# Optimization experiments

Hardware: AMD Instinct MI355X
Metric: run time of the kernel (lower is better)

Reference implementation:

```python
import jax, jax.numpy as jnp
import numpy as np

# TT config: input_dimension=2048, output_multiplier=4, rank=16
# top_ranks    = [8,2,2,2,2,2,2,2,2]  (prod = 2048)
# bottom_ranks = [8,2,2,2,2,2,2,2,2]  (prod = 2048)
# core shapes (top, bottom, left, right): left/right are TT bond ranks.
CORE_SHAPES = [(8, 8, 1, 16)] + [(2, 2, 16, 16)] * 7 + [(2, 2, 16, 1)]


def setup_inputs() -> dict:
    key = jax.random.key(0)
    ks = jax.random.split(key, 10)
    inp = {"x": jax.random.normal(ks[0], (4, 2048, 2048), dtype=jnp.float32)}
    for i, s in enumerate(CORE_SHAPES):
        inp[f"p{i}"] = jax.random.normal(ks[i + 1], s, dtype=jnp.float32)
    return inp


def _tt_apply(x, ps):
    # x: [B, S, D] with D = prod(top_ranks) = 2048
    B, S, D = x.shape
    T = B * S
    # Normalize every core to (top, bottom, left_bond_in, right_bond_out).
    # Original einsum: '... abcdefghi, ajs, bkst, cltu, dmuv, envw, fowx, gpxy, hqzy, irz -> ... jklmnopqr'
    # Core 7 ('hqzy') has swapped bonds: its 4th dim (y) is the incoming bond
    # from core 6 and its 3rd dim (z) is the outgoing bond into core 8 ('irz').
    cores = list(ps[:7]) + [jnp.transpose(ps[7], (0, 1, 3, 2)), ps[8]]
    # core 0 is used as p0[:, :, 0, :] in the original; its left dim is 1 so
    # keeping the singleton left axis is identical math.
    y = x.reshape(T, 1, 1, D)  # [T, out_so_far=1, bond=1, remaining_top=D]
    J, M = 1, D
    for g in cores:
        tk, bk, lk, rk = g.shape
        y = y.reshape(T, J, lk, tk, M // tk)
        # contract incoming bond l and current top index a with the core
        y = jnp.einsum('tjlam,ablr->tjbrm', y, g)
        J *= bk
        M //= tk
        y = y.reshape(T, J, rk, M)
    # final: rk == 1, M == 1 -> [T, J] with J = prod(bottom_ranks) = 2048
    return y.reshape(B, S, J)


def reference(x, p0, p1, p2, p3, p4, p5, p6, p7, p8):
    return _tt_apply(x, (p0, p1, p2, p3, p4, p5, p6, p7, p8))
```

## Files before the change

### kernel.cpp

```cpp
#include <hip/hip_runtime.h>
#include <stdint.h>

typedef unsigned short u16;
typedef __bf16 bf16x8 __attribute__((ext_vector_type(8)));
typedef float f32x16 __attribute__((ext_vector_type(16)));
typedef u16 u16x8 __attribute__((ext_vector_type(8)));

__device__ __forceinline__ u16 f2bf(float f) {
  uint32_t u = __float_as_uint(f);
  u += 0x7fffu + ((u >> 16) & 1u);
  return (u16)(u >> 16);
}

__global__ __launch_bounds__(256) void build_lr_kernel(
    const float* __restrict__ p0, const float* __restrict__ p1,
    const float* __restrict__ p2, const float* __restrict__ p3,
    const float* __restrict__ p4, const float* __restrict__ p5,
    const float* __restrict__ p6, const float* __restrict__ p7,
    const float* __restrict__ p8, float* __restrict__ L4, float* __restrict__ R) {
  __shared__ float sA[16384];
  __shared__ float sB[4096];
  const int tid = threadIdx.x;
  if (blockIdx.x < 16) {
    for (int i = tid; i < 1024; i += 256) sA[i] = p0[i];
    __syncthreads();
    for (int i = tid; i < 4096; i += 256) {
      int r = i & 15, t = i >> 4;
      int Bb = t & 15, Aa = t >> 4;
      int a = Aa & 1, A = Aa >> 1, b = Bb & 1, B = Bb >> 1;
      const float* srow = sA + (A * 8 + B) * 16;
      const float* g = p1 + ((a * 2 + b) * 16) * 16 + r;
      float s = 0.f;
#pragma unroll
      for (int l = 0; l < 16; l++) s += srow[l] * g[l * 16];
      sB[i] = s;
    }
    __syncthreads();
    for (int i = tid; i < 16384; i += 256) {
      int r = i & 15, t = i >> 4;
      int Bb = t & 31, Aa = t >> 5;
      int a = Aa & 1, A = Aa >> 1, b = Bb & 1, B = Bb >> 1;
      const float* srow = sB + (A * 16 + B) * 16;
      const float* g = p2 + ((a * 2 + b) * 16) * 16 + r;
      float s = 0.f;
#pragma unroll
      for (int l = 0; l < 16; l++) s += srow[l] * g[l * 16];
      sA[i] = s;
    }
    __syncthreads();
    int gi = blockIdx.x * 256 + tid;
    int b3 = gi & 1, a3 = (gi >> 1) & 1;
    int B2 = (gi >> 2) & 31, A2 = gi >> 7;
    const float* srow = sA + (A2 * 32 + B2) * 16;
    const float* g3 = p3 + ((a3 * 2 + b3) * 16) * 16;
    float tmp[16];
#pragma unroll
    for (int r3 = 0; r3 < 16; r3++) {
      float s = 0.f;
#pragma unroll
      for (int r2 = 0; r2 < 16; r2++) s += srow[r2] * g3[r2 * 16 + r3];
      tmp[r3] = s;
    }
#pragma unroll
    for (int ab = 0; ab < 4; ab++) {
      int a4 = ab >> 1, b4 = ab & 1;
      const float* g4 = p4 + (ab * 16) * 16;
      int AL = A2 * 4 + a3 * 2 + a4;
      int BL = B2 * 4 + b3 * 2 + b4;
      float* drow = L4 + (AL * 128 + BL) * 16;
#pragma unroll
      for (int r4 = 0; r4 < 16; r4++) {
        float s = 0.f;
#pragma unroll
        for (int r3 = 0; r3 < 16; r3++) s += tmp[r3] * g4[r3 * 16 + r4];
        drow[r4] = s;
      }
    }
  } else {
    for (int i = tid; i < 64; i += 256) sA[i] = p8[i];
    __syncthreads();
    for (int i = tid; i < 256; i += 256) {
      int rl = i & 15, t = i >> 4;
      int Bt = t & 3, At = t >> 2;
      int a = At >> 1, Ap = At & 1, b = Bt >> 1, Bp = Bt & 1;
      const float* srow = sA + (Ap * 2 + Bp) * 16;
      const float* g = p7 + ((a * 2 + b) * 16) * 16 + rl;
      float s = 0.f;
#pragma unroll
      for (int rk = 0; rk < 16; rk++) s += srow[rk] * g[rk * 16];
      sB[i] = s;
    }
    __syncthreads();
    for (int i = tid; i < 1024; i += 256) {
      int rl = i & 15, t = i >> 4;
      int Bt = t & 7, At = t >> 3;
      int a = At >> 2, Ap = At & 3, b = Bt >> 2, Bp = Bt & 3;
      const float* srow = sB + (Ap * 4 + Bp) * 16;
      const float* g = p6 + (((a * 2 + b) * 16) + rl) * 16;
      float s = 0.f;
#pragma unroll
      for (int rk = 0; rk < 16; rk++) s += srow[rk] * g[rk];
      sA[i] = s;
    }
    __syncthreads();
    for (int i = tid; i < 4096; i += 256) {
      int rl = i & 15, t = i >> 4;
      int Bt = t & 15, At = t >> 4;
      int a = At >> 3, Ap = At & 7, b = Bt >> 3, Bp = Bt & 7;
      const float* srow = sA + (Ap * 8 + Bp) * 16;
      const float* g = p5 + (((a * 2 + b) * 16) + rl) * 16;
      float s = 0.f;
#pragma unroll
      for (int rk = 0; rk < 16; rk++) s += srow[rk] * g[rk];
      R[i] = s;
    }
  }
}

__global__ __launch_bounds__(256) void prep_kernel(const float* __restrict__ L4,
                                                   const float* __restrict__ R,
                                                   u16* __restrict__ Wt,
                                                   const float* __restrict__ x,
                                                   u16* __restrict__ xb) {
  if (blockIdx.x < 2048) {
    int t = blockIdx.x * 256 + threadIdx.x;
    int e = t * 8;
    int Af = e & 2047;
    int Bf = e >> 11;
    const float* lrow = L4 + ((Af >> 4) * 128 + (Bf >> 4)) * 16;
    float lv[16];
#pragma unroll
    for (int r = 0; r < 16; r++) lv[r] = lrow[r];
    const float* rbase = R + (Bf & 15) * 16;
    u16x8 o;
#pragma unroll
    for (int j = 0; j < 8; j++) {
      const float* rrow = rbase + ((Af + j) & 15) * 256;
      float s = 0.f;
#pragma unroll
      for (int r = 0; r < 16; r++) s += lv[r] * rrow[r];
      o[j] = f2bf(s);
    }
    *(u16x8*)(Wt + (size_t)Bf * 2048 + Af) = o;
  } else {
    size_t i = ((size_t)(blockIdx.x - 2048) * 256 + threadIdx.x) * 8;
    float4 u = *(const float4*)(x + i);
    float4 v = *(const float4*)(x + i + 4);
    u16x8 o;
    o[0] = f2bf(u.x); o[1] = f2bf(u.y); o[2] = f2bf(u.z); o[3] = f2bf(u.w);
    o[4] = f2bf(v.x); o[5] = f2bf(v.y); o[6] = f2bf(v.z); o[7] = f2bf(v.w);
    *(u16x8*)(xb + i) = o;
  }
}

#define SB0() __builtin_amdgcn_sched_barrier(0)

#define STAGE_OP(g, S, h, dsto, gk)                                            \
  __builtin_amdgcn_global_load_lds(                                            \
      (const __attribute__((address_space(1))) void*)(g[h][0] + (gk)),         \
      (__attribute__((address_space(3))) void*)(S + (dsto) + ldst), 16, 0, 0); \
  __builtin_amdgcn_global_load_lds(                                            \
      (const __attribute__((address_space(1))) void*)(g[h][1] + (gk)),         \
      (__attribute__((address_space(3))) void*)(S + (dsto) + ldst + 4096), 16, 0, 0);

#define STAGE_A(h, dsto, gk) STAGE_OP(gA, As, h, dsto, gk)
#define STAGE_B(h, dsto, gk) STAGE_OP(gB, Bs, h, dsto, gk)

#define LOAD_AF(ah, pa)                                                        \
  _Pragma("unroll") for (int m = 0; m < 2; m++)                                \
      _Pragma("unroll") for (int ks = 0; ks < 4; ks++)                         \
          af[m][ks] = *(const bf16x8*)(As + (pa) + (ah) * 8192 + rbA +         \
                                       m * 2048 + ((((ks * 2) + hl) ^ key) * 8));

#define LOAD_BV(bh, pa)                                                        \
  _Pragma("unroll") for (int ks = 0; ks < 4; ks++)                             \
      bv[ks] = *(const bf16x8*)(Bs + (pa) + (bh) * 8192 + rbB +                \
                                ((((ks * 2) + hl) ^ key) * 8));

#define MFMA8(ah, bh)                                                          \
  _Pragma("unroll") for (int ks = 0; ks < 4; ks++) {                           \
    acc[ah][bh][0] = __builtin_amdgcn_mfma_f32_32x32x16_bf16(                  \
        af[0][ks], bv[ks], acc[ah][bh][0], 0, 0, 0);                           \
    acc[ah][bh][1] = __builtin_amdgcn_mfma_f32_32x32x16_bf16(                  \
        af[1][ks], bv[ks], acc[ah][bh][1], 0, 0, 0);                           \
  }

#define PH_MID()                                                               \
  SB0();                                                                       \
  asm volatile("s_barrier" ::: "memory");                                      \
  asm volatile("s_waitcnt lgkmcnt(0)" ::: "memory");                           \
  SB0();                                                                       \
  __builtin_amdgcn_s_setprio(1);

#define PH_END()                                                               \
  __builtin_amdgcn_s_setprio(0);                                               \
  SB0();                                                                       \
  asm volatile("s_barrier" ::: "memory");                                      \
  SB0();

#define PH_END_VM()                                                            \
  __builtin_amdgcn_s_setprio(0);                                               \
  SB0();                                                                       \
  asm volatile("s_waitcnt vmcnt(6)" ::: "memory");                             \
  asm volatile("s_barrier" ::: "memory");                                      \
  SB0();

__global__ __launch_bounds__(512, 2) void gemm_kernel(const u16* __restrict__ A,
                                                      const u16* __restrict__ B,
                                                      float* __restrict__ C) {
  __shared__ alignas(128) u16 As[4 * 8192];
  __shared__ alignas(128) u16 Bs[4 * 8192];
  const int tid = threadIdx.x;
  const int lane = tid & 63;
  const int w = tid >> 6;
  const int wr = w >> 2;
  const int wc = w & 3;
  const int r32 = lane & 31;
  const int hl = lane >> 5;

  const int F = blockIdx.x + (blockIdx.y << 3);
  const int li = F >> 3;
  const int m0 = ((F & 7) * 4 + (li >> 3)) << 8;
  const int n0 = (li & 7) << 8;

  const int srow = lane >> 3;
  const int soct = (lane & 7) ^ srow;
  const u16* gA[2][2];
  const u16* gB[2][2];
#pragma unroll
  for (int h = 0; h < 2; h++)
#pragma unroll
    for (int q = 0; q < 2; q++) {
      int r = h * 128 + q * 64 + w * 8 + srow;
      gA[h][q] = A + (size_t)(m0 + r) * 2048 + soct * 8;
      gB[h][q] = B + (size_t)(n0 + r) * 2048 + soct * 8;
    }
  const int ldst = w * 512;

  const int key = r32 & 7;
  const int rbA = (wr * 64 + r32) * 64;
  const int rbB = (wc * 32 + r32) * 64;

  f32x16 acc[2][2][2] = {};
  bf16x8 af[2][4], bv[4];

  STAGE_A(0, 0, 0);      SB0();
  STAGE_B(1, 8192, 0);   SB0();
  STAGE_A(1, 8192, 0);   SB0();
  STAGE_B(0, 0, 0);      SB0();
  STAGE_A(0, 16384, 64); SB0();
  STAGE_B(1, 24576, 64); SB0();
  STAGE_A(1, 24576, 64); SB0();
  asm volatile("s_waitcnt vmcnt(6)" ::: "memory");
  asm volatile("s_barrier" ::: "memory");
  SB0();

  for (int t = 0; t < 32; t++) {
    const int pa = (t & 1) << 14;
    const int pan = 16384 - pa;
    const int k1 = (t + 1 < 32 ? t + 1 : 31) * 64;
    const int k2 = (t + 2 < 32 ? t + 2 : 31) * 64;
    LOAD_AF(0, pa);
    LOAD_BV(0, pa);
    STAGE_B(0, pan, k1);
    PH_MID();
    MFMA8(0, 0);
    PH_END();
    LOAD_BV(1, pa);
    STAGE_A(0, pa, k2);
    PH_MID();
    MFMA8(0, 1);
    PH_END();
    LOAD_AF(1, pa);
    STAGE_B(1, pa + 8192, k2);
    PH_MID();
    MFMA8(1, 1);
    PH_END();
    LOAD_BV(0, pa);
    STAGE_A(1, pa + 8192, k2);
    PH_MID();
    MFMA8(1, 0);
    PH_END_VM();
  }

  asm volatile("s_waitcnt vmcnt(0)" ::: "memory");

#pragma unroll
  for (int ah = 0; ah < 2; ah++)
#pragma unroll
    for (int bh = 0; bh < 2; bh++)
#pragma unroll
      for (int m = 0; m < 2; m++) {
        size_t cbase = (size_t)(m0 + ah * 128 + wr * 64 + m * 32 + 4 * hl) * 2048 +
                       (n0 + bh * 128 + wc * 32 + r32);
#pragma unroll
        for (int reg = 0; reg < 16; reg++) {
          int row = (reg & 3) + 8 * (reg >> 2);
          __builtin_nontemporal_store(acc[ah][bh][m][reg], C + cbase + (size_t)row * 2048);
        }
      }
}

extern "C" void kernel_launch(void* const* d_in, const int* in_sizes, int n_in,
                              void* d_out, int out_size, void* d_ws, size_t ws_size,
                              hipStream_t stream) {
  const float* x = (const float*)d_in[0];
  const float* p0 = (const float*)d_in[1];
  const float* p1 = (const float*)d_in[2];
  const float* p2 = (const float*)d_in[3];
  const float* p3 = (const float*)d_in[4];
  const float* p4 = (const float*)d_in[5];
  const float* p5 = (const float*)d_in[6];
  const float* p6 = (const float*)d_in[7];
  const float* p7 = (const float*)d_in[8];
  const float* p8 = (const float*)d_in[9];
  char* ws = (char*)d_ws;
  u16* xbf = (u16*)ws;
  u16* Wt = (u16*)(ws + 33554432);
  float* L4 = (float*)(ws + 41943040);
  float* R = (float*)(ws + 42991616);

  build_lr_kernel<<<17, 256, 0, stream>>>(p0, p1, p2, p3, p4, p5, p6, p7, p8, L4, R);
  prep_kernel<<<10240, 256, 0, stream>>>(L4, R, Wt, x, xbf);
  gemm_kernel<<<dim3(8, 32), 512, 0, stream>>>(xbf, Wt, (float*)d_out);
}
```

Before: 271.0 us.

## Restructure GEMM main loop with double-buffered B fragments and finer LDS waits

Reworks the 4-phase GEMM K-loop so B fragments are double-buffered in registers (bv0/bv1). The next tile's first B fragment is prefetched before the end-of-iteration barrier, and partial lgkmcnt waits let MFMAs start before every LDS read has returned. Per-thread global pointer arrays are replaced by one lane offset plus uniform row offsets, which should cut VGPR use and address arithmetic. This removes some barriers and full LDS drains on the critical path, at the cost of more live fragment registers and more subtle ordering requirements between the LDS reads and the async global-to-LDS stages.

```diff
diff --git a/kernel.cpp b/kernel.cpp
--- a/kernel.cpp
+++ b/kernel.cpp
@@ -154,56 +154,42 @@
 }
 
 #define SB0() __builtin_amdgcn_sched_barrier(0)
-
-#define STAGE_OP(g, S, h, dsto, gk)                                            \
+#define LGKM(n) asm volatile("s_waitcnt lgkmcnt(" #n ")" ::: "memory")
+#define VMCW(n) asm volatile("s_waitcnt vmcnt(" #n ")" ::: "memory")
+#define BAR() asm volatile("s_barrier" ::: "memory")
+
+#define STAGE1(Sbase, dsto, gp, uoff)                                          \
   __builtin_amdgcn_global_load_lds(                                            \
-      (const __attribute__((address_space(1))) void*)(g[h][0] + (gk)),         \
-      (__attribute__((address_space(3))) void*)(S + (dsto) + ldst), 16, 0, 0); \
-  __builtin_amdgcn_global_load_lds(                                            \
-      (const __attribute__((address_space(1))) void*)(g[h][1] + (gk)),         \
-      (__attribute__((address_space(3))) void*)(S + (dsto) + ldst + 4096), 16, 0, 0);
-
-#define STAGE_A(h, dsto, gk) STAGE_OP(gA, As, h, dsto, gk)
-#define STAGE_B(h, dsto, gk) STAGE_OP(gB, Bs, h, dsto, gk)
-
-#define LOAD_AF(ah, pa)                                                        \
-  _Pragma("unroll") for (int m = 0; m < 2; m++)                                \
-      _Pragma("unroll") for (int ks = 0; ks < 4; ks++)                         \
-          af[m][ks] = *(const bf16x8*)(As + (pa) + (ah) * 8192 + rbA +         \
-                                       m * 2048 + ((((ks * 2) + hl) ^ key) * 8));
-
-#define LOAD_BV(bh, pa)                                                        \
+      (const __attribute__((address_space(1))) void*)((gp) + (uoff) + pl),     \
+      (__attribute__((address_space(3))) void*)((Sbase) + (dsto) + ldst), 16, 0, 0)
+
+#define STAGE_A(h, dsto, gk)                                                   \
+  STAGE1(As, (dsto), A, uA + ((h)*128) * 2048 + (gk));                         \
+  STAGE1(As, (dsto) + 4096, A, uA + ((h)*128 + 64) * 2048 + (gk))
+
+#define STAGE_B(h, dsto, gk)                                                   \
+  STAGE1(Bs, (dsto), B, uB + ((h)*128) * 2048 + (gk));                         \
+  STAGE1(Bs, (dsto) + 4096, B, uB + ((h)*128 + 64) * 2048 + (gk))
+
+#define LOAD_AF_H(dst, ah, m, pav)                                             \
   _Pragma("unroll") for (int ks = 0; ks < 4; ks++)                             \
-      bv[ks] = *(const bf16x8*)(Bs + (pa) + (bh) * 8192 + rbB +                \
-                                ((((ks * 2) + hl) ^ key) * 8));
-
-#define MFMA8(ah, bh)                                                          \
+      dst[ks] = *(const bf16x8*)(As + (pav) + (ah)*8192 + rbA + (m)*2048 +     \
+                                 (((ks * 2 + hl) ^ key) * 8))
+
+#define LOAD_BV(dst, bh, pav)                                                  \
+  _Pragma("unroll") for (int ks = 0; ks < 4; ks++)                             \
+      dst[ks] = *(const bf16x8*)(Bs + (pav) + (bh)*8192 + rbB +                \
+                                 (((ks * 2 + hl) ^ key) * 8))
+
+#define MFMA4(afh, bvv, accv)                                                  \
+  _Pragma("unroll") for (int ks = 0; ks < 4; ks++)                             \
+      accv = __builtin_amdgcn_mfma_f32_32x32x16_bf16(afh[ks], bvv[ks], accv, 0, 0, 0)
+
+#define MFMA8I(afarr, bvv, accp)                                               \
   _Pragma("unroll") for (int ks = 0; ks < 4; ks++) {                           \
-    acc[ah][bh][0] = __builtin_amdgcn_mfma_f32_32x32x16_bf16(                  \
-        af[0][ks], bv[ks], acc[ah][bh][0], 0, 0, 0);                           \
-    acc[ah][bh][1] = __builtin_amdgcn_mfma_f32_32x32x16_bf16(                  \
-        af[1][ks], bv[ks], acc[ah][bh][1], 0, 0, 0);                           \
+    accp[0] = __builtin_amdgcn_mfma_f32_32x32x16_bf16(afarr[0][ks], bvv[ks], accp[0], 0, 0, 0); \
+    accp[1] = __builtin_amdgcn_mfma_f32_32x32x16_bf16(afarr[1][ks], bvv[ks], accp[1], 0, 0, 0); \
   }
-
-#define PH_MID()                                                               \
-  SB0();                                                                       \
-  asm volatile("s_barrier" ::: "memory");                                      \
-  asm volatile("s_waitcnt lgkmcnt(0)" ::: "memory");                           \
-  SB0();                                                                       \
-  __builtin_amdgcn_s_setprio(1);
-
-#define PH_END()                                                               \
-  __builtin_amdgcn_s_setprio(0);                                               \
-  SB0();                                                                       \
-  asm volatile("s_barrier" ::: "memory");                                      \
-  SB0();
-
-#define PH_END_VM()                                                            \
-  __builtin_amdgcn_s_setprio(0);                                               \
-  SB0();                                                                       \
-  asm volatile("s_waitcnt vmcnt(6)" ::: "memory");                             \
-  asm volatile("s_barrier" ::: "memory");                                      \
-  SB0();
 
 __global__ __launch_bounds__(512, 2) void gemm_kernel(const u16* __restrict__ A,
                                                       const u16* __restrict__ B,
@@ -225,16 +211,9 @@
 
   const int srow = lane >> 3;
   const int soct = (lane & 7) ^ srow;
-  const u16* gA[2][2];
-  const u16* gB[2][2];
-#pragma unroll
-  for (int h = 0; h < 2; h++)
-#pragma unroll
-    for (int q = 0; q < 2; q++) {
-      int r = h * 128 + q * 64 + w * 8 + srow;
-      gA[h][q] = A + (size_t)(m0 + r) * 2048 + soct * 8;
-      gB[h][q] = B + (size_t)(n0 + r) * 2048 + soct * 8;
-    }
+  const int uA = m0 * 2048;
+  const int uB = n0 * 2048;
+  const int pl = (w * 8 + srow) * 2048 + soct * 8;
   const int ldst = w * 512;
 
   const int key = r32 & 7;
@@ -242,7 +221,7 @@
   const int rbB = (wc * 32 + r32) * 64;
 
   f32x16 acc[2][2][2] = {};
-  bf16x8 af[2][4], bv[4];
+  bf16x8 af[2][4], bv0[4], bv1[4];
 
   STAGE_A(0, 0, 0);      SB0();
   STAGE_B(1, 8192, 0);   SB0();
@@ -251,39 +230,58 @@
   STAGE_A(0, 16384, 64); SB0();
   STAGE_B(1, 24576, 64); SB0();
   STAGE_A(1, 24576, 64); SB0();
-  asm volatile("s_waitcnt vmcnt(6)" ::: "memory");
-  asm volatile("s_barrier" ::: "memory");
+  VMCW(6);
+  BAR();
+  LOAD_BV(bv0, 0, 0);
   SB0();
 
+#pragma unroll 1
   for (int t = 0; t < 32; t++) {
-    const int pa = (t & 1) << 14;
-    const int pan = 16384 - pa;
-    const int k1 = (t + 1 < 32 ? t + 1 : 31) * 64;
-    const int k2 = (t + 2 < 32 ? t + 2 : 31) * 64;
-    LOAD_AF(0, pa);
-    LOAD_BV(0, pa);
-    STAGE_B(0, pan, k1);
-    PH_MID();
-    MFMA8(0, 0);
-    PH_END();
-    LOAD_BV(1, pa);
-    STAGE_A(0, pa, k2);
-    PH_MID();
-    MFMA8(0, 1);
-    PH_END();
-    LOAD_AF(1, pa);
-    STAGE_B(1, pa + 8192, k2);
-    PH_MID();
-    MFMA8(1, 1);
-    PH_END();
-    LOAD_BV(0, pa);
-    STAGE_A(1, pa + 8192, k2);
-    PH_MID();
-    MFMA8(1, 0);
-    PH_END_VM();
+    const int pav = (t & 1) << 14;
+    const int pnv = 16384 - pav;
+    const int k1 = (t < 31 ? t + 1 : 31) * 64;
+    const int k2 = (t < 30 ? t + 2 : 31) * 64;
+    STAGE_B(0, pnv, k1);
+    SB0();
+    LOAD_AF_H(af[0], 0, 0, pav); SB0();
+    LOAD_AF_H(af[1], 0, 1, pav); SB0();
+    LOAD_BV(bv1, 1, pav);
+    LGKM(8); SB0();
+    __builtin_amdgcn_s_setprio(1);
+    MFMA4(af[0], bv0, acc[0][0][0]);
+    LGKM(4); SB0();
+    MFMA4(af[1], bv0, acc[0][0][1]);
+    __builtin_amdgcn_s_setprio(0);
+    BAR();
+    STAGE_A(0, pav, k2);
+    LGKM(0); SB0();
+    __builtin_amdgcn_s_setprio(1);
+    MFMA8I(af, bv1, acc[0][1]);
+    __builtin_amdgcn_s_setprio(0);
+    BAR();
+    STAGE_B(1, pav + 8192, k2);
+    SB0();
+    LOAD_AF_H(af[0], 1, 0, pav); SB0();
+    LOAD_AF_H(af[1], 1, 1, pav);
+    LGKM(4); SB0();
+    __builtin_amdgcn_s_setprio(1);
+    MFMA4(af[0], bv1, acc[1][1][0]);
+    LGKM(0); SB0();
+    MFMA4(af[1], bv1, acc[1][1][1]);
+    __builtin_amdgcn_s_setprio(0);
+    BAR();
+    STAGE_A(1, pav + 8192, k2);
+    SB0();
+    __builtin_amdgcn_s_setprio(1);
+    MFMA8I(af, bv0, acc[1][0]);
+    __builtin_amdgcn_s_setprio(0);
+    VMCW(6);
+    BAR();
+    LOAD_BV(bv0, 0, pnv);
+    SB0();
   }
 
-  asm volatile("s_waitcnt vmcnt(0)" ::: "memory");
+  VMCW(0);
 
 #pragma unroll
   for (int ah = 0; ah < 2; ah++)
```

New measurement: 270.3 us. No clear change (-0.3%).
